# Performance work log

Hardware: AMD Instinct MI355X
Metric: run time of the kernel (lower is better)

The kernel has to match this reference:

```python
import jax, jax.numpy as jnp
import numpy as np

PATCH_SIZE = 16


def setup_inputs() -> dict:
    key = jax.random.key(0)
    images = jax.random.normal(key, (64, 384, 384, 3), dtype=jnp.float32)
    return {"images": images}


def reference(images) -> jnp.ndarray:
    # images: [B, H, W, 3], channels-last. Extract non-overlapping PxP patches
    # and flatten each (row-major over (P, P, 3), matching torch.flatten).
    b, h, w, c = images.shape
    p = PATCH_SIZE
    g = h // p  # grid size
    # [B, G, P, G, P, C] -> [B, G, G, P, P, C] -> [B, G*G, P*P*C]
    x = images.reshape(b, g, p, g, p, c)
    x = x.transpose(0, 1, 3, 2, 4, 5)
    return x.reshape(b, g * g, p * p * c)
```

## Files before the change

### kernel.cpp

```cpp
#include <hip/hip_runtime.h>


typedef float f4 __attribute__((ext_vector_type(4)));

constexpr int Bsz = 64;
constexpr int Hh  = 384;
constexpr int Ww  = 384;
constexpr int C   = 3;
constexpr int P   = 16;
constexpr int G   = 24;
constexpr int ROW4   = Ww * C / 4;
constexpr int CHUNK4 = P * C / 4;
constexpr int TOT4   = Bsz * G * G * P * CHUNK4;
constexpr int ELEMS  = 4;
constexpr int NTHREADS = TOT4 / ELEMS;

__global__ __launch_bounds__(256)
void patches_kernel(const f4* __restrict__ in, f4* __restrict__ out) {
    int tid = blockIdx.x * blockDim.x + threadIdx.x;

#pragma unroll
    for (int e = 0; e < ELEMS; ++e) {
        int idx = tid + e * NTHREADS;

        int k  = idx % CHUNK4;
        int t  = idx / CHUNK4;
        int py = t % P;   t /= P;
        int gx = t % G;   t /= G;
        int gy = t % G;
        int b  = t / G;

        int row  = b * Hh + gy * P + py;
        int iidx = row * ROW4 + gx * CHUNK4 + k;

        f4 v = __builtin_nontemporal_load(in + iidx);
        __builtin_nontemporal_store(v, out + idx);
    }
}

extern "C" void kernel_launch(void* const* d_in, const int* in_sizes, int n_in,
                              void* d_out, int out_size, void* d_ws, size_t ws_size,
                              hipStream_t stream) {
    const f4* in  = (const f4*)d_in[0];
    f4*       out = (f4*)d_out;

    constexpr int BLOCK = 256;
    constexpr int GRID  = NTHREADS / BLOCK;
    patches_kernel<<<GRID, BLOCK, 0, stream>>>(in, out);
}
```

Measured before the change: 193.0 us.

## Stage half-patch-row slabs through LDS for coalesced loads and stores

Each block now loads an 8-row by full-width slab of the image with fully contiguous vector loads, writes it to padded shared memory, then reads it back in output order so the stores go out as 192-float4 contiguous runs per patch. Before, each thread gathered 12-float4 chunks directly. The goal is longer contiguous memory transactions on both sides. The cost is an LDS round trip, a barrier, and 36 float4 registers per thread, which may cut occupancy.

```diff
diff --git a/kernel.cpp b/kernel.cpp
--- a/kernel.cpp
+++ b/kernel.cpp
@@ -3,38 +3,58 @@
 
 typedef float f4 __attribute__((ext_vector_type(4)));
 
-constexpr int Bsz = 64;
-constexpr int Hh  = 384;
-constexpr int Ww  = 384;
-constexpr int C   = 3;
-constexpr int P   = 16;
-constexpr int G   = 24;
-constexpr int ROW4   = Ww * C / 4;
-constexpr int CHUNK4 = P * C / 4;
-constexpr int TOT4   = Bsz * G * G * P * CHUNK4;
-constexpr int ELEMS  = 4;
-constexpr int NTHREADS = TOT4 / ELEMS;
+constexpr int C     = 3;
+constexpr int P     = 16;
+constexpr int G     = 24;
+constexpr int ROW4  = 384 * C / 4;
+constexpr int IMG4  = 384 * ROW4;
+constexpr int HR    = 8;
+constexpr int TILE4 = HR * ROW4;
+constexpr int LSTR  = ROW4 + 1;
+constexpr int BLOCK = 256;
+constexpr int PT    = TILE4 / BLOCK;
+constexpr int NSLAB = 64 * G * 2;
 
-__global__ __launch_bounds__(256)
+constexpr int GY4   = G * P * P * C / 4;
+constexpr int HALF4 = HR * P * C / 4;
+
+__global__ __launch_bounds__(BLOCK)
 void patches_kernel(const f4* __restrict__ in, f4* __restrict__ out) {
-    int tid = blockIdx.x * blockDim.x + threadIdx.x;
+    __shared__ f4 lds[HR * LSTR];
+
+    const int s    = blockIdx.x;
+    const int half = s & 1;
+    const int bg   = s >> 1;
+    const int gy   = bg % G;
+    const int b    = bg / G;
+    const int t    = threadIdx.x;
+
+    const int in_base  = b * IMG4 + (gy * P + half * HR) * ROW4;
+    const int out_base = b * IMG4 + gy * GY4 + half * HALF4;
+
+    f4 v[PT];
+#pragma unroll
+    for (int j = 0; j < PT; ++j)
+        v[j] = __builtin_nontemporal_load(in + in_base + t + j * BLOCK);
 
 #pragma unroll
-    for (int e = 0; e < ELEMS; ++e) {
-        int idx = tid + e * NTHREADS;
+    for (int j = 0; j < PT; ++j) {
+        int i   = t + j * BLOCK;
+        int row = i / ROW4;
+        int col = i - row * ROW4;
+        lds[row * LSTR + col] = v[j];
+    }
+    __syncthreads();
 
-        int k  = idx % CHUNK4;
-        int t  = idx / CHUNK4;
-        int py = t % P;   t /= P;
-        int gx = t % G;   t /= G;
-        int gy = t % G;
-        int b  = t / G;
-
-        int row  = b * Hh + gy * P + py;
-        int iidx = row * ROW4 + gx * CHUNK4 + k;
-
-        f4 v = __builtin_nontemporal_load(in + iidx);
-        __builtin_nontemporal_store(v, out + idx);
+#pragma unroll
+    for (int j = 0; j < PT; ++j) {
+        int o  = t + j * BLOCK;
+        int gx = o / 96;
+        int w  = o - gx * 96;
+        int py = w / 12;
+        int k  = w - py * 12;
+        f4 u = lds[py * LSTR + gx * 12 + k];
+        __builtin_nontemporal_store(u, out + out_base + gx * 192 + w);
     }
 }
 
@@ -43,8 +63,5 @@
                               hipStream_t stream) {
     const f4* in  = (const f4*)d_in[0];
     f4*       out = (f4*)d_out;
-
-    constexpr int BLOCK = 256;
-    constexpr int GRID  = NTHREADS / BLOCK;
-    patches_kernel<<<GRID, BLOCK, 0, stream>>>(in, out);
+    patches_kernel<<<NSLAB, BLOCK, 0, stream>>>(in, out);
 }
```

After: 186.0 us. 1.04x faster.

## Stage patch rows through per-wave LDS tiles with float2 accesses

Applied to the files above, without the earlier changes.

Each wavefront loads two full image rows of one half-width as contiguous float2 reads, writes them into a padded per-wave LDS buffer, then reads back in patch order and writes contiguous 24-float2 output runs. This replaces the direct float4 gather, whose reads and writes cover 12-vector (192-byte) chunks scattered across rows, with fully contiguous global accesses on both sides. It adds an LDS round trip and narrows the vector width from 16-byte to 8-byte accesses, which may increase the instruction count. The launch bounds also request higher occupancy.

```diff
diff --git a/kernel.cpp b/kernel.cpp
--- a/kernel.cpp
+++ b/kernel.cpp
@@ -1,50 +1,67 @@
 #include <hip/hip_runtime.h>
 
 
-typedef float f4 __attribute__((ext_vector_type(4)));
+typedef float f2 __attribute__((ext_vector_type(2)));
 
-constexpr int Bsz = 64;
-constexpr int Hh  = 384;
-constexpr int Ww  = 384;
-constexpr int C   = 3;
-constexpr int P   = 16;
-constexpr int G   = 24;
-constexpr int ROW4   = Ww * C / 4;
-constexpr int CHUNK4 = P * C / 4;
-constexpr int TOT4   = Bsz * G * G * P * CHUNK4;
-constexpr int ELEMS  = 4;
-constexpr int NTHREADS = TOT4 / ELEMS;
+constexpr int ROW2   = 576;
+constexpr int IMG2   = 384 * ROW2;
+constexpr int GY2    = 24 * 384;
+constexpr int LSTR2  = 289;
+constexpr int LWAVE2 = 2 * LSTR2;
+constexpr int BLOCK  = 256;
+constexpr int NTILE  = 64 * 24 * 8 * 2;
+constexpr int GRIDN  = NTILE / 4;
 
-__global__ __launch_bounds__(256)
-void patches_kernel(const f4* __restrict__ in, f4* __restrict__ out) {
-    int tid = blockIdx.x * blockDim.x + threadIdx.x;
+__global__ __launch_bounds__(BLOCK, 8)
+void patches_kernel(const f2* __restrict__ in, f2* __restrict__ out) {
+    __shared__ f2 lds[4 * LWAVE2];
+    const int wv = threadIdx.x >> 6;
+    const int l  = threadIdx.x & 63;
+    f2* __restrict__ L = &lds[wv * LWAVE2];
+
+    const int tau = blockIdx.x * 4 + wv;
+    const int h   = tau & 1;
+    const int t1  = tau >> 1;
+    const int p   = t1 & 7;
+    const int t2  = t1 >> 3;
+    const int gy  = t2 % 24;
+    const int b   = t2 / 24;
+
+    const f2* ibase = in + b * IMG2 + (gy * 16 + 2 * p) * ROW2 + h * 288;
+    f2 v[9];
+#pragma unroll
+    for (int j = 0; j < 9; ++j) {
+        int i  = l + j * 64;
+        int r  = (i >= 288) ? 1 : 0;
+        int c2 = i - r * 288;
+        v[j] = __builtin_nontemporal_load(ibase + r * ROW2 + c2);
+    }
 
 #pragma unroll
-    for (int e = 0; e < ELEMS; ++e) {
-        int idx = tid + e * NTHREADS;
+    for (int j = 0; j < 9; ++j) {
+        int i  = l + j * 64;
+        int r  = (i >= 288) ? 1 : 0;
+        int c2 = i - r * 288;
+        L[r * LSTR2 + c2] = v[j];
+    }
 
-        int k  = idx % CHUNK4;
-        int t  = idx / CHUNK4;
-        int py = t % P;   t /= P;
-        int gx = t % G;   t /= G;
-        int gy = t % G;
-        int b  = t / G;
-
-        int row  = b * Hh + gy * P + py;
-        int iidx = row * ROW4 + gx * CHUNK4 + k;
-
-        f4 v = __builtin_nontemporal_load(in + iidx);
-        __builtin_nontemporal_store(v, out + idx);
+    f2* obase = out + b * IMG2 + gy * GY2 + h * (12 * 384) + p * 48;
+#pragma unroll
+    for (int j = 0; j < 9; ++j) {
+        int o   = l + j * 64;
+        int gxl = o / 48;
+        int w   = o - gxl * 48;
+        int py2 = (w >= 24) ? 1 : 0;
+        int w2  = w - py2 * 24;
+        f2 x = L[py2 * LSTR2 + gxl * 24 + w2];
+        __builtin_nontemporal_store(x, obase + gxl * 384 + py2 * 24 + w2);
     }
 }
 
 extern "C" void kernel_launch(void* const* d_in, const int* in_sizes, int n_in,
                               void* d_out, int out_size, void* d_ws, size_t ws_size,
                               hipStream_t stream) {
-    const f4* in  = (const f4*)d_in[0];
-    f4*       out = (f4*)d_out;
-
-    constexpr int BLOCK = 256;
-    constexpr int GRID  = NTHREADS / BLOCK;
-    patches_kernel<<<GRID, BLOCK, 0, stream>>>(in, out);
+    const f2* in  = (const f2*)d_in[0];
+    f2*       out = (f2*)d_out;
+    patches_kernel<<<GRIDN, BLOCK, 0, stream>>>(in, out);
 }
```

Result: faster. 186.6 us (-3.3%).
